# Kernel optimization log

Hardware: AMD Instinct MI355X
Metric: run time of the kernel (lower is better)

The kernel has to match this reference:

```python
import jax, jax.numpy as jnp
import numpy as np

T, B, A, OBS = 128, 16, 32, 256
K, NACT, HID = 3, 9, 32


def setup_inputs() -> dict:
    key = jax.random.key(0)
    ks = jax.random.split(key, 12)
    sc = 0.1  # small init scale for stability
    d = {}
    d["x"] = jax.random.normal(ks[0], (T, B, A, OBS), jnp.float32)
    d["done"] = jax.random.randint(ks[1], (T, B), 0, 2, jnp.int32)
    d["actions"] = jax.random.randint(ks[2], (T, B, A, K), 0, NACT, jnp.int32)
    d["W1"] = sc * jax.random.normal(ks[3], (128, OBS), jnp.float32)
    d["b1"] = jnp.zeros((128,), jnp.float32)
    d["W2"] = sc * jax.random.normal(ks[4], (128, 128), jnp.float32)
    d["b2"] = jnp.zeros((128,), jnp.float32)
    d["W3"] = sc * jax.random.normal(ks[5], (64, 128), jnp.float32)
    d["b3"] = jnp.zeros((64,), jnp.float32)
    d["Wih"] = sc * jax.random.normal(ks[6], (4 * HID, 64), jnp.float32)
    d["Whh"] = sc * jax.random.normal(ks[7], (4 * HID, HID), jnp.float32)
    d["bih"] = jnp.zeros((4 * HID,), jnp.float32)
    d["bhh"] = jnp.zeros((4 * HID,), jnp.float32)
    d["Wh"] = sc * jax.random.normal(ks[8], (K, NACT, HID), jnp.float32)
    d["bh"] = jnp.zeros((K, NACT), jnp.float32)
    d["h0"] = jnp.zeros((B * A, HID), jnp.float32)
    d["c0"] = jnp.zeros((B * A, HID), jnp.float32)
    return d


def _forward(x, done, actions, W1, b1, W2, b2, W3, b3,
             Wih, Whh, bih, bhh, Wh, bh, h0, c0):
    # MLP trunk: n_obs -> 128 -> 128 -> 64 (tanh, tanh, linear)
    z = jnp.tanh(x @ W1.T + b1)
    z = jnp.tanh(z @ W2.T + b2)
    z = z @ W3.T + b3                       # [T, B, A, 64]
    zf = z.reshape(T, B * A, 64)
    # done[t] repeated per agent (repeat_interleave along batch*agent axis)
    done_f = jnp.repeat(done.astype(x.dtype), A, axis=1)  # [T, B*A]

    def step(carry, inp):
        h, c = carry
        zt, dt = inp                        # [B*A,64], [B*A]
        mask = (1.0 - dt)[:, None]
        h = h * mask
        c = c * mask
        gates = zt @ Wih.T + bih + h @ Whh.T + bhh  # [B*A, 4H]
        i, f, g, o = jnp.split(gates, 4, axis=-1)   # PyTorch gate order i,f,g,o
        i, f, o = jax.nn.sigmoid(i), jax.nn.sigmoid(f), jax.nn.sigmoid(o)
        g = jnp.tanh(g)
        c = f * c + i * g
        h = o * jnp.tanh(c)
        return (h, c), h

    (_, _), ys = jax.lax.scan(step, (h0, c0), (zf, done_f))
    y = ys.reshape(T, B, A, HID)
    # multi-head categorical logits: stacked heads [K, NACT, HID]
    logits = jnp.einsum('tbah,knh->tbakn', y, Wh) + bh  # [T,B,A,K,NACT]
    lp = jax.nn.log_softmax(logits, axis=-1)
    entropies = -jnp.sum(jnp.exp(lp) * lp, axis=-1)     # [T,B,A,K]
    alp = jnp.take_along_axis(lp, actions[..., None], axis=-1)[..., 0]  # [T,B,A,K]
    logprobs = jnp.prod(alp, axis=-1)  # faithful: product of per-head log-probs
    return logprobs, entropies


def reference(x, done, actions, W1, b1, W2, b2, W3, b3,
              Wih, Whh, bih, bhh, Wh, bh, h0, c0):
    logprobs, entropies = _forward(x, done, actions, W1, b1, W2, b2, W3, b3,
                                   Wih, Whh, bih, bhh, Wh, bh, h0, c0)
    return actions, logprobs, entropies
```

## Files before the change

### kernel.cpp

```cpp
#include <hip/hip_runtime.h>
#include <math.h>

namespace {
constexpr int Tn = 128, Bn = 16, An = 32, OBS = 256, Kh = 3, NACT = 9, HID = 32;
constexpr int TBA = Tn * Bn * An;
constexpr int BA  = Bn * An;
constexpr int OUT_LP  = TBA * Kh;
constexpr int OUT_ENT = TBA * Kh + TBA;

constexpr int W1_OFF  = 0;
constexpr int W2_OFF  = 32768;
constexpr int W3_OFF  = 49152;
constexpr int WIH_OFF = 57344;
constexpr int W16_TOT = 65536;

typedef __fp16   pk16x2 __attribute__((ext_vector_type(2)));
typedef _Float16 half8v __attribute__((ext_vector_type(8)));
typedef float    f32x4  __attribute__((ext_vector_type(4)));
}

__device__ __forceinline__ float fast_sig(float x) {
  return __builtin_amdgcn_rcpf(1.f + __expf(-x));
}
__device__ __forceinline__ float fast_tanh(float x) {
  return fmaf(2.f, fast_sig(2.f * x), -1.f);
}
__device__ __forceinline__ unsigned h2bits(pk16x2 h) {
  return __builtin_bit_cast(unsigned, h);
}
__device__ __forceinline__ pk16x2 bits2h(unsigned u) {
  return __builtin_bit_cast(pk16x2, u);
}
__device__ __forceinline__ float dot2(pk16x2 a, pk16x2 b, float c) {
#if __has_builtin(__builtin_amdgcn_fdot2)
  return __builtin_amdgcn_fdot2(a, b, c, false);
#else
  c = fmaf((float)a.x, (float)b.x, c);
  return fmaf((float)a.y, (float)b.y, c);
#endif
}
__device__ __forceinline__ float dpp_swap1(float x) {
  return __uint_as_float((unsigned)__builtin_amdgcn_mov_dpp(
      (int)__float_as_uint(x), 0xB1, 0xF, 0xF, true));
}

__global__ __launch_bounds__(256) void cvtw_kernel(
    const float* __restrict__ W1, const float* __restrict__ W2,
    const float* __restrict__ W3, const float* __restrict__ Wih,
    _Float16* __restrict__ w16)
{
  int i = blockIdx.x * 256 + threadIdx.x;
  float v;
  if (i < W2_OFF)       v = W1[i];
  else if (i < W3_OFF)  v = W2[i - W2_OFF];
  else if (i < WIH_OFF) v = W3[i - W3_OFF];
  else                  v = Wih[i - WIH_OFF];
  w16[i] = (_Float16)v;
}

template<int ROWS, int WSTR>
__device__ __forceinline__ void stage_wh(const _Float16* __restrict__ Wg, int kofs,
                                         _Float16* __restrict__ wt, int tid)
{
#pragma unroll
  for (int it = 0; it < ROWS/32; ++it) {
    int idx = tid + it*256;
    int o = idx >> 3, g8 = idx & 7;
    *(half8v*)&wt[o*72 + g8*8] =
        *(const half8v*)&Wg[(size_t)o*WSTR + kofs + g8*8];
  }
}

template<int NOC, int XSTR>
__device__ __forceinline__ void mfma_slab(const _Float16* __restrict__ xsrc,
                                          const _Float16* __restrict__ wt,
                                          int rA, int ln, int quad, f32x4 acc[8])
{
#pragma unroll
  for (int kc = 0; kc < 2; ++kc) {
    half8v a = *(const half8v*)&xsrc[rA*XSTR + kc*32 + quad*8];
#pragma unroll
    for (int oc = 0; oc < NOC; ++oc) {
      half8v b = *(const half8v*)&wt[(oc*16 + ln)*72 + kc*32 + quad*8];
      acc[oc] = __builtin_amdgcn_mfma_f32_16x16x32_f16(a, b, acc[oc], 0, 0, 0);
    }
  }
}

__global__ __launch_bounds__(256) void mlp_kernel(
    const float* __restrict__ x, const _Float16* __restrict__ w16,
    const float* __restrict__ b1, const float* __restrict__ b2,
    const float* __restrict__ b3, const float* __restrict__ bih,
    const float* __restrict__ bhh, uint2* __restrict__ G1q)
{
  __shared__ __align__(16) _Float16 xs[64*72];
  __shared__ __align__(16) _Float16 wt[128*72];
  __shared__ __align__(16) _Float16 act[64*136];
  const _Float16* W1h  = w16 + W1_OFF;
  const _Float16* W2h  = w16 + W2_OFF;
  const _Float16* W3h  = w16 + W3_OFF;
  const _Float16* Wihh = w16 + WIH_OFF;
  const int tid  = threadIdx.x;
  const int w    = tid >> 6;
  const int lane = tid & 63;
  const int ln   = lane & 15;
  const int quad = lane >> 4;
  const int rA   = 16*w + ln;
  const int r0   = 16*w + quad*4;
  const int R0   = blockIdx.x * 64;
  f32x4 acc[8];

#pragma unroll
  for (int oc = 0; oc < 8; ++oc) acc[oc] = (f32x4)0.f;
  for (int kt = 0; kt < 4; ++kt) {
#pragma unroll
    for (int it = 0; it < 2; ++it) {
      int idx = tid + it*256;
      int r = idx >> 3, g8 = idx & 7;
      const float* xp = &x[(size_t)(R0 + r)*OBS + kt*64 + g8*8];
      float4 v0 = *(const float4*)xp;
      float4 v1 = *(const float4*)(xp + 4);
      half8v hv = { (_Float16)v0.x, (_Float16)v0.y, (_Float16)v0.z, (_Float16)v0.w,
                    (_Float16)v1.x, (_Float16)v1.y, (_Float16)v1.z, (_Float16)v1.w };
      *(half8v*)&xs[r*72 + g8*8] = hv;
    }
    stage_wh<128, 256>(W1h, kt*64, wt, tid);
    __syncthreads();
    mfma_slab<8, 72>(xs, wt, rA, ln, quad, acc);
    __syncthreads();
  }
#pragma unroll
  for (int oc = 0; oc < 8; ++oc) {
    int o = oc*16 + ln;
    float bv = b1[o];
#pragma unroll
    for (int r = 0; r < 4; ++r)
      act[(r0 + r)*136 + o] = (_Float16)fast_tanh(acc[oc][r] + bv);
  }

#pragma unroll
  for (int oc = 0; oc < 8; ++oc) acc[oc] = (f32x4)0.f;
  for (int kt = 0; kt < 2; ++kt) {
    stage_wh<128, 128>(W2h, kt*64, wt, tid);
    __syncthreads();
    mfma_slab<8, 136>(act + kt*64, wt, rA, ln, quad, acc);
    __syncthreads();
  }
#pragma unroll
  for (int oc = 0; oc < 8; ++oc) {
    int o = oc*16 + ln;
    float bv = b2[o];
#pragma unroll
    for (int r = 0; r < 4; ++r)
      act[(r0 + r)*136 + o] = (_Float16)fast_tanh(acc[oc][r] + bv);
  }

#pragma unroll
  for (int oc = 0; oc < 4; ++oc) acc[oc] = (f32x4)0.f;
  for (int kt = 0; kt < 2; ++kt) {
    stage_wh<64, 128>(W3h, kt*64, wt, tid);
    __syncthreads();
    mfma_slab<4, 136>(act + kt*64, wt, rA, ln, quad, acc);
    __syncthreads();
  }
#pragma unroll
  for (int oc = 0; oc < 4; ++oc) {
    int o = oc*16 + ln;
    float bv = b3[o];
#pragma unroll
    for (int r = 0; r < 4; ++r)
      xs[(r0 + r)*72 + o] = (_Float16)(acc[oc][r] + bv);
  }

#pragma unroll
  for (int oc = 0; oc < 8; ++oc) acc[oc] = (f32x4)0.f;
  stage_wh<128, 64>(Wihh, 0, wt, tid);
  __syncthreads();
  mfma_slab<8, 72>(xs, wt, rA, ln, quad, acc);
#pragma unroll
  for (int p = 0; p < 2; ++p) {
    int ui = p*16 + ln;
    float bi = bih[ui]      + bhh[ui];
    float bf = bih[ui + 32] + bhh[ui + 32];
    float bg = bih[ui + 64] + bhh[ui + 64];
    float bo = bih[ui + 96] + bhh[ui + 96];
#pragma unroll
    for (int r = 0; r < 4; ++r) {
      int n = R0 + r0 + r;
      uint2 q;
      q.x = h2bits(__builtin_amdgcn_cvt_pkrtz(acc[p  ][r] + bi, acc[p+4][r] + bg));
      q.y = h2bits(__builtin_amdgcn_cvt_pkrtz(acc[p+2][r] + bf, acc[p+6][r] + bo));
      G1q[(size_t)n*32 + ui] = q;
    }
  }
}

__global__ __launch_bounds__(64) void lstm_kernel(
    const uint2* __restrict__ G1q, const float* __restrict__ Whh,
    const int* __restrict__ done, const float* __restrict__ h0,
    const float* __restrict__ c0, unsigned* __restrict__ Y16)
{
  const int lane = threadIdx.x;
  const int u = lane & 31;
  const int row = blockIdx.x;
  const int b = row >> 5;

  pk16x2 wi[16], wf[16], wg[16], wo[16];
#pragma unroll
  for (int k4 = 0; k4 < 8; ++k4) {
    float4 a  = *(const float4*)&Whh[(u      )*HID + k4*4];
    float4 bq = *(const float4*)&Whh[(u + 32 )*HID + k4*4];
    float4 cq = *(const float4*)&Whh[(u + 64 )*HID + k4*4];
    float4 dq = *(const float4*)&Whh[(u + 96 )*HID + k4*4];
    wi[2*k4+0] = __builtin_amdgcn_cvt_pkrtz(a.x,  a.y);
    wi[2*k4+1] = __builtin_amdgcn_cvt_pkrtz(a.z,  a.w);
    wf[2*k4+0] = __builtin_amdgcn_cvt_pkrtz(bq.x, bq.y);
    wf[2*k4+1] = __builtin_amdgcn_cvt_pkrtz(bq.z, bq.w);
    wg[2*k4+0] = __builtin_amdgcn_cvt_pkrtz(cq.x, cq.y);
    wg[2*k4+1] = __builtin_amdgcn_cvt_pkrtz(cq.z, cq.w);
    wo[2*k4+0] = __builtin_amdgcn_cvt_pkrtz(dq.x, dq.y);
    wo[2*k4+1] = __builtin_amdgcn_cvt_pkrtz(dq.z, dq.w);
  }

  unsigned long long dm0 = __ballot(done[lane*Bn + b] != 0);
  unsigned long long dm1 = __ballot(done[(lane + 64)*Bn + b] != 0);

  float c = c0[row*HID + u];
  float h = h0[row*HID + u];
  unsigned pk = h2bits(__builtin_amdgcn_cvt_pkrtz(h, dpp_swap1(h)));

  const uint2* gbase = G1q + (size_t)row*32 + u;
  const size_t gstride = (size_t)BA*32;
  uint2 q0 = gbase[0*gstride];
  uint2 q1 = gbase[1*gstride];
  uint2 q2 = gbase[2*gstride];
  uint2 q3 = gbase[3*gstride];

#define LSTM_PHASE(TT, Q)                                                \
  {                                                                      \
    uint2 cur = Q;                                                       \
    int tnx = (TT) + 4; tnx = (tnx < Tn) ? tnx : (Tn - 1);               \
    Q = gbase[(size_t)tnx * gstride];                                    \
    unsigned long long dbit = ((TT) < 64) ? (dm0 >> (TT))                \
                                          : (dm1 >> ((TT) - 64));        \
    float m = (dbit & 1ull) ? 0.f : 1.f;         \
    unsigned hp[16];                                                     \
    _Pragma("unroll") for (int k = 0; k < 16; ++k)                       \
      hp[k] = __builtin_amdgcn_readlane(pk, 2*k);                        \
    float ai0=0.f, ai1=0.f, af0=0.f, af1=0.f;                            \
    float ag0=0.f, ag1=0.f, ao0=0.f, ao1=0.f;                            \
    _Pragma("unroll") for (int k = 0; k < 16; k += 2) {                  \
      pk16x2 ha = bits2h(hp[k]), hb = bits2h(hp[k+1]);                   \
      ai0 = dot2(wi[k], ha, ai0); ai1 = dot2(wi[k+1], hb, ai1);          \
      af0 = dot2(wf[k], ha, af0); af1 = dot2(wf[k+1], hb, af1);          \
      ag0 = dot2(wg[k], ha, ag0); ag1 = dot2(wg[k+1], hb, ag1);          \
      ao0 = dot2(wo[k], ha, ao0); ao1 = dot2(wo[k+1], hb, ao1);          \
    }                                                                    \
    pk16x2 ig = bits2h(cur.x), fo = bits2h(cur.y);                       \
    float gi = fmaf(m, ai0 + ai1, (float)ig.x);                          \
    float gf = fmaf(m, af0 + af1, (float)fo.x);                          \
    float gg = fmaf(m, ag0 + ag1, (float)ig.y);                          \
    float go = fmaf(m, ao0 + ao1, (float)fo.y);                          \
    float iv = fast_sig(gi), fv = fast_sig(gf);                          \
    float gv = fast_tanh(gg), ov = fast_sig(go);                         \
    c = fmaf(fv, m * c, iv * gv);                                        \
    h = ov * fast_tanh(c);                                               \
    pk = h2bits(__builtin_amdgcn_cvt_pkrtz(h, dpp_swap1(h)));            \
    if ((lane & 33) == 0)                                                \
      Y16[((size_t)(TT)*BA + row)*16 + (u >> 1)] = pk;                   \
  }

  for (int t = 0; t < Tn; t += 4) {
    LSTM_PHASE(t + 0, q0)
    LSTM_PHASE(t + 1, q1)
    LSTM_PHASE(t + 2, q2)
    LSTM_PHASE(t + 3, q3)
  }
#undef LSTM_PHASE
}

__global__ __launch_bounds__(256) void head_kernel(
    const unsigned* __restrict__ Y16, const float* __restrict__ Wh,
    const float* __restrict__ bh, const int* __restrict__ actions,
    float* __restrict__ out)
{
  __shared__ __align__(16) float whs[27*32];
  __shared__ float bhs[32];
  const int tid = threadIdx.x;
  const int R0 = blockIdx.x * 256;
  for (int i = tid; i < 27*32; i += 256) whs[i] = Wh[i];
  if (tid < 27) bhs[tid] = bh[tid];
  const int row = R0 + tid;
  float yv[32];
#pragma unroll
  for (int i4 = 0; i4 < 4; ++i4) {
    uint4 yw = *(const uint4*)&Y16[(size_t)row*16 + i4*4];
    pk16x2 p0 = bits2h(yw.x), p1 = bits2h(yw.y), p2 = bits2h(yw.z), p3 = bits2h(yw.w);
    yv[i4*8+0] = (float)p0.x; yv[i4*8+1] = (float)p0.y;
    yv[i4*8+2] = (float)p1.x; yv[i4*8+3] = (float)p1.y;
    yv[i4*8+4] = (float)p2.x; yv[i4*8+5] = (float)p2.y;
    yv[i4*8+6] = (float)p3.x; yv[i4*8+7] = (float)p3.y;
  }
  __syncthreads();
  float l[27];
#pragma unroll
  for (int m = 0; m < 27; ++m) {
    float a = bhs[m];
#pragma unroll
    for (int k4 = 0; k4 < 8; ++k4) {
      float4 w4 = *(const float4*)&whs[m*32 + k4*4];
      a = fmaf(yv[k4*4+0], w4.x, a);
      a = fmaf(yv[k4*4+1], w4.y, a);
      a = fmaf(yv[k4*4+2], w4.z, a);
      a = fmaf(yv[k4*4+3], w4.w, a);
    }
    l[m] = a;
  }
  float logprob = 1.0f;
#pragma unroll
  for (int kk = 0; kk < 3; ++kk) {
    float mx = l[kk*9];
#pragma unroll
    for (int n = 1; n < 9; ++n) mx = fmaxf(mx, l[kk*9+n]);
    float s = 0.f;
#pragma unroll
    for (int n = 0; n < 9; ++n) s += __expf(l[kk*9+n] - mx);
    float lse = mx + __logf(s);
    float ent = 0.f;
#pragma unroll
    for (int n = 0; n < 9; ++n) {
      float lp = l[kk*9+n] - lse;
      ent -= __expf(lp) * lp;
    }
    int a = actions[row*3 + kk];
    float alp = 0.f;
#pragma unroll
    for (int n = 0; n < 9; ++n) alp = (a == n) ? (l[kk*9+n] - lse) : alp;
    logprob *= alp;
    out[row*3 + kk] = (float)a;
    out[OUT_ENT + row*3 + kk] = ent;
  }
  out[OUT_LP + row] = logprob;
}

extern "C" void kernel_launch(void* const* d_in, const int* in_sizes, int n_in,
                              void* d_out, int out_size, void* d_ws, size_t ws_size,
                              hipStream_t stream)
{
  const float* x       = (const float*)d_in[0];
  const int*   done    = (const int*)  d_in[1];
  const int*   actions = (const int*)  d_in[2];
  const float* W1  = (const float*)d_in[3];
  const float* b1  = (const float*)d_in[4];
  const float* W2  = (const float*)d_in[5];
  const float* b2  = (const float*)d_in[6];
  const float* W3  = (const float*)d_in[7];
  const float* b3  = (const float*)d_in[8];
  const float* Wih = (const float*)d_in[9];
  const float* Whh = (const float*)d_in[10];
  const float* bih = (const float*)d_in[11];
  const float* bhh = (const float*)d_in[12];
  const float* Wh  = (const float*)d_in[13];
  const float* bh  = (const float*)d_in[14];
  const float* h0  = (const float*)d_in[15];
  const float* c0  = (const float*)d_in[16];
  float* out = (float*)d_out;

  uint2* G1q = (uint2*)d_ws;
  unsigned* Y16 = (unsigned*)(G1q + (size_t)TBA*32);
  _Float16* W16 = (_Float16*)(Y16 + (size_t)TBA*16);

  cvtw_kernel<<<W16_TOT/256, 256, 0, stream>>>(W1, W2, W3, Wih, W16);
  mlp_kernel<<<TBA/64, 256, 0, stream>>>(x, W16, b1, b2, b3, bih, bhh, G1q);
  lstm_kernel<<<BA, 64, 0, stream>>>(G1q, Whh, done, h0, c0, Y16);
  head_kernel<<<TBA/256, 256, 0, stream>>>(Y16, Wh, bh, actions, out);
}
```

Measured before the change: 198.9 us.

## Fuse categorical head into LSTM kernel and fold action copy into weight conversion

Moves the multi-head logits, log-softmax, entropy and log-prob computation into the sequential LSTM kernel. Each step evaluates the head for the previous timestep's hidden state, using lanes as (head, action) pairs with DPP reductions, so the Y16 intermediate buffer and the separate head kernel go away. The actions-to-float output copy is appended as extra blocks to the weight conversion kernel. The trade-off is extra per-step work and global stores on the latency-bound recurrent critical path of 512 single-wave blocks.

Result: slower. 222.2 us (+11.7%).

```diff
diff --git a/kernel.cpp b/kernel.cpp
--- a/kernel.cpp
+++ b/kernel.cpp
@@ -39,23 +39,42 @@
   return fmaf((float)a.y, (float)b.y, c);
 #endif
 }
-__device__ __forceinline__ float dpp_swap1(float x) {
+template<int CTRL>
+__device__ __forceinline__ float dpp_movf(float x) {
   return __uint_as_float((unsigned)__builtin_amdgcn_mov_dpp(
-      (int)__float_as_uint(x), 0xB1, 0xF, 0xF, true));
-}
-
-__global__ __launch_bounds__(256) void cvtw_kernel(
+      (int)__float_as_uint(x), CTRL, 0xF, 0xF, true));
+}
+__device__ __forceinline__ float dpp_swap1(float x) { return dpp_movf<0xB1>(x); }
+__device__ __forceinline__ float dpp_sum16(float v) {
+  v += dpp_movf<0xB1>(v);  v += dpp_movf<0x4E>(v);
+  v += dpp_movf<0x124>(v); v += dpp_movf<0x128>(v);
+  return v;
+}
+__device__ __forceinline__ float dpp_max16(float v) {
+  v = fmaxf(v, dpp_movf<0xB1>(v));  v = fmaxf(v, dpp_movf<0x4E>(v));
+  v = fmaxf(v, dpp_movf<0x124>(v)); v = fmaxf(v, dpp_movf<0x128>(v));
+  return v;
+}
+
+__global__ __launch_bounds__(256) void cvtw_act_kernel(
     const float* __restrict__ W1, const float* __restrict__ W2,
     const float* __restrict__ W3, const float* __restrict__ Wih,
-    _Float16* __restrict__ w16)
-{
-  int i = blockIdx.x * 256 + threadIdx.x;
-  float v;
-  if (i < W2_OFF)       v = W1[i];
-  else if (i < W3_OFF)  v = W2[i - W2_OFF];
-  else if (i < WIH_OFF) v = W3[i - W3_OFF];
-  else                  v = Wih[i - WIH_OFF];
-  w16[i] = (_Float16)v;
+    _Float16* __restrict__ w16, const int* __restrict__ actions,
+    float* __restrict__ out)
+{
+  const int bid = blockIdx.x;
+  if (bid < W16_TOT/256) {
+    int i = bid * 256 + threadIdx.x;
+    float v;
+    if (i < W2_OFF)       v = W1[i];
+    else if (i < W3_OFF)  v = W2[i - W2_OFF];
+    else if (i < WIH_OFF) v = W3[i - W3_OFF];
+    else                  v = Wih[i - WIH_OFF];
+    w16[i] = (_Float16)v;
+  } else {
+    int i = (bid - W16_TOT/256) * 256 + threadIdx.x;
+    out[i] = (float)actions[i];
+  }
 }
 
 template<int ROWS, int WSTR>
@@ -195,10 +214,12 @@
   }
 }
 
-__global__ __launch_bounds__(64) void lstm_kernel(
+__global__ __launch_bounds__(64) void lstm_head_kernel(
     const uint2* __restrict__ G1q, const float* __restrict__ Whh,
     const int* __restrict__ done, const float* __restrict__ h0,
-    const float* __restrict__ c0, unsigned* __restrict__ Y16)
+    const float* __restrict__ c0, const int* __restrict__ actions,
+    const float* __restrict__ Wh, const float* __restrict__ bh,
+    float* __restrict__ out)
 {
   const int lane = threadIdx.x;
   const int u = lane & 31;
@@ -222,6 +243,21 @@
     wo[2*k4+1] = __builtin_amdgcn_cvt_pkrtz(dq.z, dq.w);
   }
 
+  const int hk = lane >> 4;
+  const int hj = lane & 15;
+  const bool jvalid = (hj < 9) && (hk < 3);
+  const int wk = jvalid ? hk : 0;
+  const int wj = jvalid ? hj : 0;
+  const float* whrow = Wh + (size_t)(wk*NACT + wj)*HID;
+  pk16x2 whp[16];
+#pragma unroll
+  for (int p = 0; p < 8; ++p) {
+    float4 v = *(const float4*)&whrow[p*4];
+    whp[2*p+0] = __builtin_amdgcn_cvt_pkrtz(v.x, v.y);
+    whp[2*p+1] = __builtin_amdgcn_cvt_pkrtz(v.z, v.w);
+  }
+  const float bhv = jvalid ? bh[wk*NACT + wj] : 0.f;
+
   unsigned long long dm0 = __ballot(done[lane*Bn + b] != 0);
   unsigned long long dm1 = __ballot(done[(lane + 64)*Bn + b] != 0);
 
@@ -235,6 +271,38 @@
   uint2 q1 = gbase[1*gstride];
   uint2 q2 = gbase[2*gstride];
   uint2 q3 = gbase[3*gstride];
+
+#define HEAD_STEP(TM1)                                                     \
+  {                                                                        \
+    const int tm1 = (TM1);                                                 \
+    const int nprev = tm1*BA + row;                                        \
+    const int nld = (tm1 < 0) ? row : nprev;                               \
+    int av = actions[(size_t)nld*3 + ((lane < 3) ? lane : 0)];             \
+    int a0 = __builtin_amdgcn_readlane(av, 0);                             \
+    int a1 = __builtin_amdgcn_readlane(av, 1);                             \
+    int a2 = __builtin_amdgcn_readlane(av, 2);                             \
+    int ak = (hk == 0) ? a0 : ((hk == 1) ? a1 : a2);                       \
+    float lg = bhv;                                                        \
+    _Pragma("unroll") for (int p = 0; p < 16; ++p)                         \
+      lg = dot2(whp[p], bits2h(hp[p]), lg);                                \
+    lg = jvalid ? lg : -3.0e38f;                                           \
+    float mx = dpp_max16(lg);                                              \
+    float e = jvalid ? __expf(lg - mx) : 0.f;                              \
+    float s = dpp_sum16(e);                                                \
+    float lse = mx + __logf(s);                                            \
+    float rs = __builtin_amdgcn_rcpf(s);                                   \
+    float lp = lg - lse;                                                   \
+    float ent = dpp_sum16(e * rs * lp);                                    \
+    float alp = dpp_sum16((jvalid && (hj == ak)) ? lp : 0.f);              \
+    float pa = __uint_as_float(__builtin_amdgcn_readlane(__float_as_uint(alp), 0));  \
+    float pb = __uint_as_float(__builtin_amdgcn_readlane(__float_as_uint(alp), 16)); \
+    float pc = __uint_as_float(__builtin_amdgcn_readlane(__float_as_uint(alp), 32)); \
+    if (tm1 >= 0) {                                                        \
+      if ((hj == 0) && (hk < 3))                                           \
+        out[OUT_ENT + (size_t)nprev*3 + hk] = -ent;                        \
+      if (lane == 0) out[OUT_LP + nprev] = pa * pb * pc;                   \
+    }                                                                      \
+  }
 
 #define LSTM_PHASE(TT, Q)                                                \
   {                                                                      \
@@ -266,8 +334,7 @@
     c = fmaf(fv, m * c, iv * gv);                                        \
     h = ov * fast_tanh(c);                                               \
     pk = h2bits(__builtin_amdgcn_cvt_pkrtz(h, dpp_swap1(h)));            \
-    if ((lane & 33) == 0)                                                \
-      Y16[((size_t)(TT)*BA + row)*16 + (u >> 1)] = pk;                   \
+    HEAD_STEP((TT) - 1)                                                  \
   }
 
   for (int t = 0; t < Tn; t += 4) {
@@ -276,71 +343,16 @@
     LSTM_PHASE(t + 2, q2)
     LSTM_PHASE(t + 3, q3)
   }
+
+  {
+    unsigned hp[16];
+#pragma unroll
+    for (int k = 0; k < 16; ++k)
+      hp[k] = __builtin_amdgcn_readlane(pk, 2*k);
+    HEAD_STEP(Tn - 1)
+  }
 #undef LSTM_PHASE
-}
-
-__global__ __launch_bounds__(256) void head_kernel(
-    const unsigned* __restrict__ Y16, const float* __restrict__ Wh,
-    const float* __restrict__ bh, const int* __restrict__ actions,
-    float* __restrict__ out)
-{
-  __shared__ __align__(16) float whs[27*32];
-  __shared__ float bhs[32];
-  const int tid = threadIdx.x;
-  const int R0 = blockIdx.x * 256;
-  for (int i = tid; i < 27*32; i += 256) whs[i] = Wh[i];
-  if (tid < 27) bhs[tid] = bh[tid];
-  const int row = R0 + tid;
-  float yv[32];
-#pragma unroll
-  for (int i4 = 0; i4 < 4; ++i4) {
-    uint4 yw = *(const uint4*)&Y16[(size_t)row*16 + i4*4];
-    pk16x2 p0 = bits2h(yw.x), p1 = bits2h(yw.y), p2 = bits2h(yw.z), p3 = bits2h(yw.w);
-    yv[i4*8+0] = (float)p0.x; yv[i4*8+1] = (float)p0.y;
-    yv[i4*8+2] = (float)p1.x; yv[i4*8+3] = (float)p1.y;
-    yv[i4*8+4] = (float)p2.x; yv[i4*8+5] = (float)p2.y;
-    yv[i4*8+6] = (float)p3.x; yv[i4*8+7] = (float)p3.y;
-  }
-  __syncthreads();
-  float l[27];
-#pragma unroll
-  for (int m = 0; m < 27; ++m) {
-    float a = bhs[m];
-#pragma unroll
-    for (int k4 = 0; k4 < 8; ++k4) {
-      float4 w4 = *(const float4*)&whs[m*32 + k4*4];
-      a = fmaf(yv[k4*4+0], w4.x, a);
-      a = fmaf(yv[k4*4+1], w4.y, a);
-      a = fmaf(yv[k4*4+2], w4.z, a);
-      a = fmaf(yv[k4*4+3], w4.w, a);
-    }
-    l[m] = a;
-  }
-  float logprob = 1.0f;
-#pragma unroll
-  for (int kk = 0; kk < 3; ++kk) {
-    float mx = l[kk*9];
-#pragma unroll
-    for (int n = 1; n < 9; ++n) mx = fmaxf(mx, l[kk*9+n]);
-    float s = 0.f;
-#pragma unroll
-    for (int n = 0; n < 9; ++n) s += __expf(l[kk*9+n] - mx);
-    float lse = mx + __logf(s);
-    float ent = 0.f;
-#pragma unroll
-    for (int n = 0; n < 9; ++n) {
-      float lp = l[kk*9+n] - lse;
-      ent -= __expf(lp) * lp;
-    }
-    int a = actions[row*3 + kk];
-    float alp = 0.f;
-#pragma unroll
-    for (int n = 0; n < 9; ++n) alp = (a == n) ? (l[kk*9+n] - lse) : alp;
-    logprob *= alp;
-    out[row*3 + kk] = (float)a;
-    out[OUT_ENT + row*3 + kk] = ent;
-  }
-  out[OUT_LP + row] = logprob;
+#undef HEAD_STEP
 }
 
 extern "C" void kernel_launch(void* const* d_in, const int* in_sizes, int n_in,
@@ -367,11 +379,11 @@
   float* out = (float*)d_out;
 
   uint2* G1q = (uint2*)d_ws;
-  unsigned* Y16 = (unsigned*)(G1q + (size_t)TBA*32);
-  _Float16* W16 = (_Float16*)(Y16 + (size_t)TBA*16);
-
-  cvtw_kernel<<<W16_TOT/256, 256, 0, stream>>>(W1, W2, W3, Wih, W16);
+  _Float16* W16 = (_Float16*)(G1q + (size_t)TBA*32);
+
+  cvtw_act_kernel<<<W16_TOT/256 + (TBA*Kh)/256, 256, 0, stream>>>(
+      W1, W2, W3, Wih, W16, actions, out);
   mlp_kernel<<<TBA/64, 256, 0, stream>>>(x, W16, b1, b2, b3, bih, bhh, G1q);
-  lstm_kernel<<<BA, 64, 0, stream>>>(G1q, Whh, done, h0, c0, Y16);
-  head_kernel<<<TBA/256, 256, 0, stream>>>(Y16, Wh, bh, actions, out);
-}
+  lstm_head_kernel<<<BA, 64, 0, stream>>>(G1q, Whh, done, h0, c0,
+                                          actions, Wh, bh, out);
+}
```
